# Optimization experiments

Measured on AMD Instinct MI355X. Metric: run time of the kernel, lower is better.

Reference implementation:

```python
import jax, jax.numpy as jnp
import numpy as np
import math

D_MODEL = 1024
NHEAD = 16
NUM_CLUSTERS = 32
L, N, S = 2048, 2, 2048
LN_EPS = 1e-5


def setup_inputs() -> dict:
    key = jax.random.key(0)
    ks = jax.random.split(key, 16)
    E = D_MODEL
    s = 1.0 / math.sqrt(E)
    cq = jax.random.normal(ks[0], (NUM_CLUSTERS, E), jnp.float32)
    cq = cq / jnp.linalg.norm(cq, axis=1, keepdims=True)
    ck = jax.random.normal(ks[1], (NUM_CLUSTERS, E), jnp.float32)
    ck = ck / jnp.linalg.norm(ck, axis=1, keepdims=True)
    return {
        "query": jax.random.normal(ks[2], (L, N, E), jnp.float32),
        "key": jax.random.normal(ks[3], (S, N, E), jnp.float32),
        "value": jax.random.normal(ks[4], (S, N, E), jnp.float32),
        "Wq": jax.random.uniform(ks[5], (E, E), jnp.float32, -s, s),
        "bq": jax.random.uniform(ks[6], (E,), jnp.float32, -s, s),
        "Wk": jax.random.uniform(ks[7], (E, E), jnp.float32, -s, s),
        "bk": jax.random.uniform(ks[8], (E,), jnp.float32, -s, s),
        "Wv": jax.random.uniform(ks[9], (E, E), jnp.float32, -s, s),
        "bv": jax.random.uniform(ks[10], (E,), jnp.float32, -s, s),
        "Wo": jax.random.uniform(ks[11], (E, E), jnp.float32, -s, s),
        "bo": jax.random.uniform(ks[12], (E,), jnp.float32, -s, s),
        "centroids_q": cq,
        "centroids_k": ck,
        "ln_gamma": jnp.ones((E,), jnp.float32),
        "ln_beta": jnp.zeros((E,), jnp.float32),
    }


def _assign(x, centroids):
    # spherical k-means assignment: argmax cosine similarity
    xn = x / jnp.clip(jnp.linalg.norm(x, axis=-1, keepdims=True), 1e-12)
    return jnp.argmax(xn @ centroids.T, axis=-1)


def reference(query, key, value, Wq, bq, Wk, bk, Wv, bv, Wo, bo,
              centroids_q, centroids_k, ln_gamma, ln_beta):
    Lq, Nb, E = query.shape
    Sk = key.shape[0]
    H, dh = NHEAD, E // NHEAD

    Q = query @ Wq.T + bq            # [L,N,E]
    K = key @ Wk.T + bk              # [S,N,E]
    V = value @ Wv.T + bv            # [S,N,E]

    Qb = jnp.transpose(Q, (1, 0, 2))  # [N,L,E]
    Kb = jnp.transpose(K, (1, 0, 2))  # [N,S,E]
    Vb = jnp.transpose(V, (1, 0, 2))  # [N,S,E]

    q_clusters = _assign(Qb, centroids_q)  # [N,L] int
    k_clusters = _assign(Kb, centroids_k)  # [N,S] int
    # bipartite cluster-equality mask, broadcast over heads
    mask = q_clusters[:, :, None] == k_clusters[:, None, :]  # [N,L,S]

    Qh = Qb.reshape(Nb, Lq, H, dh)
    Kh = Kb.reshape(Nb, Sk, H, dh)
    Vh = Vb.reshape(Nb, Sk, H, dh)

    scores = jnp.einsum('nlhd,nshd->nhls', Qh, Kh) / math.sqrt(dh)
    scores = jnp.where(mask[:, None, :, :], scores, -jnp.inf)
    attn = jax.nn.softmax(scores, axis=-1)  # dropout = identity (eval)

    ctx = jnp.einsum('nhls,nshd->nlhd', attn, Vh).reshape(Nb, Lq, E)
    out = ctx @ Wo.T + bo                     # [N,L,E]
    out = jnp.transpose(out, (1, 0, 2))       # [L,N,E]

    res = query + out
    mu = jnp.mean(res, axis=-1, keepdims=True)
    var = jnp.mean(jnp.square(res - mu), axis=-1, keepdims=True)
    return (res - mu) / jnp.sqrt(var + LN_EPS) * ln_gamma + ln_beta
```

## Files before the change

### kernel.cpp

```cpp
#include <hip/hip_runtime.h>
#include <stdint.h>

#define L_SEQ 2048
#define S_SEQ 2048
#define NB 2
#define EMB 1024
#define NH 16
#define DH 64
#define NC 32
#define MROWS 4096

typedef __bf16 bf16x8 __attribute__((ext_vector_type(8)));
typedef float f32x4 __attribute__((ext_vector_type(4)));

__device__ __forceinline__ float bf2f(unsigned short u) {
  return __builtin_bit_cast(float, (uint32_t)u << 16);
}
__device__ __forceinline__ unsigned short f2bf(float f) {
  uint32_t u = __builtin_bit_cast(uint32_t, f);
  return (unsigned short)((u + 0x7FFFu + ((u >> 16) & 1u)) >> 16);
}

#if defined(__has_builtin) && __has_builtin(__builtin_amdgcn_global_load_lds)
#define GLOAD_LDS(gp, lp)                                            \
  __builtin_amdgcn_global_load_lds(                                  \
      (const __attribute__((address_space(1))) void*)(gp),           \
      (__attribute__((address_space(3))) void*)(lp), 16, 0, 0)
#else
#define GLOAD_LDS(gp, lp) do { *(uint4*)(lp) = *(const uint4*)(gp); } while (0)
#endif

__global__ void __launch_bounds__(256) conv_f2bf_kernel(
    const float* __restrict__ src, unsigned short* __restrict__ dst, int n8)
{
  int id = blockIdx.x * 256 + threadIdx.x;
  if (id >= n8) return;
  const float4* s = (const float4*)src + (size_t)id * 2;
  float4 a0 = s[0], a1 = s[1];
  uint4 u;
  u.x = (uint32_t)f2bf(a0.x) | ((uint32_t)f2bf(a0.y) << 16);
  u.y = (uint32_t)f2bf(a0.z) | ((uint32_t)f2bf(a0.w) << 16);
  u.z = (uint32_t)f2bf(a1.x) | ((uint32_t)f2bf(a1.y) << 16);
  u.w = (uint32_t)f2bf(a1.z) | ((uint32_t)f2bf(a1.w) << 16);
  ((uint4*)dst)[id] = u;
}

__global__ void __launch_bounds__(256) gemm_bt_mfma(
    const unsigned short* __restrict__ A, const unsigned short* __restrict__ B,
    const float* __restrict__ bias,
    float* __restrict__ outF, unsigned short* __restrict__ outB)
{
  __shared__ __align__(16) unsigned short As[128][32];
  __shared__ __align__(16) unsigned short Bs[128][32];
  const int K = EMB;
  int tid = threadIdx.x;
  int m0 = blockIdx.y * 128, n0 = blockIdx.x * 128;
  int wave = tid >> 6, lane = tid & 63;
  int wm = (wave >> 1) * 64, wn = (wave & 1) * 64;

  f32x4 zero = {0.f, 0.f, 0.f, 0.f};
  f32x4 acc[4][4];
#pragma unroll
  for (int mi = 0; mi < 4; mi++)
#pragma unroll
    for (int ni = 0; ni < 4; ni++) acc[mi][ni] = zero;

  int fr = lane & 15, fk = (lane >> 4) * 8;

  for (int k0 = 0; k0 < K; k0 += 32) {
    __syncthreads();
#pragma unroll
    for (int it = 0; it < 2; it++) {
      int ch = tid + it * 256;
      int row = ch >> 2, kk = (ch & 3) * 8;
      GLOAD_LDS(A + (size_t)(m0 + row) * K + k0 + kk, &As[row][kk]);
      GLOAD_LDS(B + (size_t)(n0 + row) * K + k0 + kk, &Bs[row][kk]);
    }
    __syncthreads();
    bf16x8 af[4], bfr[4];
#pragma unroll
    for (int i = 0; i < 4; i++) af[i] = *(const bf16x8*)(&As[wm + i * 16 + fr][fk]);
#pragma unroll
    for (int i = 0; i < 4; i++) bfr[i] = *(const bf16x8*)(&Bs[wn + i * 16 + fr][fk]);
#pragma unroll
    for (int mi = 0; mi < 4; mi++)
#pragma unroll
      for (int ni = 0; ni < 4; ni++)
        acc[mi][ni] = __builtin_amdgcn_mfma_f32_16x16x32_bf16(af[mi], bfr[ni], acc[mi][ni], 0, 0, 0);
  }

#pragma unroll
  for (int ni = 0; ni < 4; ni++) {
    int col = n0 + wn + ni * 16 + (lane & 15);
    float bv = bias[col];
#pragma unroll
    for (int mi = 0; mi < 4; mi++) {
#pragma unroll
      for (int r = 0; r < 4; r++) {
        int row = m0 + wm + mi * 16 + (lane >> 4) * 4 + r;
        float v = acc[mi][ni][r] + bv;
        if (outF) outF[(size_t)row * EMB + col] = v;
        else outB[(size_t)row * EMB + col] = f2bf(v);
      }
    }
  }
}

__global__ void __launch_bounds__(256) prep_partial_kernel(
    const float* __restrict__ Wq_, const float* __restrict__ cq_,
    const float* __restrict__ Wk_, const float* __restrict__ ck_,
    double* __restrict__ partQ, double* __restrict__ partK)
{
  const float* W; const float* cent; double* part;
  if (blockIdx.z == 0) { W = Wq_; cent = cq_; part = partQ; }
  else                 { W = Wk_; cent = ck_; part = partK; }
  int tid = threadIdx.x;
  int k = (blockIdx.y << 6) | (tid & 63);
  int cbase = __builtin_amdgcn_readfirstlane(tid >> 6) * 8;
  int e0 = blockIdx.x << 6;

  double acc[8];
#pragma unroll
  for (int j = 0; j < 8; j++) acc[j] = 0.0;

#pragma unroll 2
  for (int e = 0; e < 64; e++) {
    double w = (double)W[(size_t)(e0 + e) * EMB + k];
#pragma unroll
    for (int j = 0; j < 8; j++)
      acc[j] += w * (double)cent[(size_t)(cbase + j) * EMB + e0 + e];
  }
#pragma unroll
  for (int j = 0; j < 8; j++)
    part[((size_t)blockIdx.x * NC + cbase + j) * EMB + k] = acc[j];
}

__global__ void __launch_bounds__(256) prep_reduce_kernel(
    const double* __restrict__ partQ, const double* __restrict__ partK,
    double* __restrict__ WcTq, double* __restrict__ WcTk)
{
  int id = blockIdx.x * 256 + threadIdx.x;
  const double* part; double* WcT; int local;
  if (id < NC * EMB) { part = partQ; WcT = WcTq; local = id; }
  else               { part = partK; WcT = WcTk; local = id - NC * EMB; }
  int c = local >> 10, k = local & 1023;
  double s = 0.0;
  for (int es = 0; es < 16; es++)
    s += part[((size_t)es * NC + c) * EMB + k];
  WcT[(size_t)k * NC + c] = s;
}

__global__ void __launch_bounds__(256) prep_bd_kernel(
    const float* __restrict__ bq_, const float* __restrict__ cq_,
    const float* __restrict__ bk_, const float* __restrict__ ck_,
    double* __restrict__ bdq, double* __restrict__ bdk)
{
  const float* bias; const float* cent; double* bd;
  if (blockIdx.x == 0) { bias = bq_; cent = cq_; bd = bdq; }
  else                 { bias = bk_; cent = ck_; bd = bdk; }
  int tid = threadIdx.x;
  int c = tid & 31, g = tid >> 5;
  __shared__ double red[8][32];
  double s2 = 0.0;
  for (int e = g * 128; e < (g + 1) * 128; e++)
    s2 += (double)bias[e] * (double)cent[(size_t)c * EMB + e];
  red[g][c] = s2;
  __syncthreads();
  if (tid < 32) {
    double t = 0.0;
#pragma unroll
    for (int gg = 0; gg < 8; gg++) t += red[gg][tid];
    bd[tid] = t;
  }
}

__global__ void __launch_bounds__(256, 2) assign2_kernel(
    const float* __restrict__ Xq, const double* __restrict__ WcTq, const double* __restrict__ bdq,
    int* __restrict__ qcl, int* __restrict__ qcnt,
    const float* __restrict__ Xk, const double* __restrict__ WcTk, const double* __restrict__ bdk,
    int* __restrict__ kcl, int* __restrict__ kcnt)
{
  const float* X; const double* WcT; const double* bd; int* cluster; int* count;
  if (blockIdx.y == 0) { X = Xq; WcT = WcTq; bd = bdq; cluster = qcl; count = qcnt; }
  else                 { X = Xk; WcT = WcTk; bd = bdk; cluster = kcl; count = kcnt; }

  int r0 = blockIdx.x * 16;
  int tid = threadIdx.x;
  int c = tid & 31, g = tid >> 5;

  __shared__ __align__(16) double Ws[64][32];
  __shared__ __align__(16) double Xd[16][64];

  double aAe = 0, aAo = 0, aBe = 0, aBo = 0;

  for (int k0 = 0; k0 < EMB; k0 += 64) {
    __syncthreads();
#pragma unroll
    for (int it = 0; it < 8; it++) {
      int idx = it * 256 + tid;
      ((double*)Ws)[idx] = WcT[(size_t)k0 * NC + idx];
    }
#pragma unroll
    for (int it = 0; it < 2; it++) {
      int idx = it * 256 + tid;
      int r = idx >> 5, kp = idx & 31;
      float2 xv = *(const float2*)(X + (size_t)(r0 + r) * EMB + k0 + kp * 2);
      double2 xd; xd.x = (double)xv.x; xd.y = (double)xv.y;
      *(double2*)(&Xd[r][kp * 2]) = xd;
    }
    __syncthreads();
#pragma unroll
    for (int kk = 0; kk < 64; kk += 2) {
      double w0 = Ws[kk][c], w1 = Ws[kk + 1][c];
      double2 xa = *(const double2*)(&Xd[g * 2][kk]);
      double2 xb = *(const double2*)(&Xd[g * 2 + 1][kk]);
      aAe += xa.x * w0; aAo += xa.y * w1;
      aBe += xb.x * w0; aBo += xb.y * w1;
    }
  }

  double dA = (aAe + aAo) + bd[c];
  double dB = (aBe + aBo) + bd[c];

  double bvA = dA; int biA = c;
  double bvB = dB; int biB = c;
#pragma unroll
  for (int off = 1; off < 32; off <<= 1) {
    double ovA = __shfl_xor(bvA, off, 64); int oiA = __shfl_xor(biA, off, 64);
    if (ovA > bvA || (ovA == bvA && oiA < biA)) { bvA = ovA; biA = oiA; }
    double ovB = __shfl_xor(bvB, off, 64); int oiB = __shfl_xor(biB, off, 64);
    if (ovB > bvB || (ovB == bvB && oiB < biB)) { bvB = ovB; biB = oiB; }
  }
  if (c == 0) {
    int rowA = r0 + g * 2, rowB = rowA + 1;
    cluster[rowA] = biA; atomicAdd(&count[(rowA & 1) * NC + biA], 1);
    cluster[rowB] = biB; atomicAdd(&count[(rowB & 1) * NC + biB], 1);
  }
}

__global__ void scan_kernel(const int* __restrict__ qcount, const int* __restrict__ kcount,
                            int* __restrict__ qoff, int* __restrict__ koff)
{
  int tid = threadIdx.x;
  if (tid < 2) {
    int run = 0;
    for (int c = 0; c < NC; c++) { qoff[tid * NC + c] = run; run += qcount[tid * NC + c]; }
  } else if (tid < 4) {
    int n = tid - 2, run = 0;
    for (int c = 0; c < NC; c++) { koff[n * NC + c] = run; run += kcount[n * NC + c]; }
  }
}

__global__ void __launch_bounds__(256) scatter_kernel(
    const int* __restrict__ q_cluster, const int* __restrict__ k_cluster,
    const int* __restrict__ qoff, const int* __restrict__ koff,
    int* __restrict__ qfill, int* __restrict__ kfill,
    int* __restrict__ qlist, int* __restrict__ klist)
{
  int id = blockIdx.x * 256 + threadIdx.x;
  if (id < MROWS) {
    int row = id, n = row & 1, l = row >> 1, c = q_cluster[row];
    int pos = atomicAdd(&qfill[n * NC + c], 1);
    qlist[n * L_SEQ + qoff[n * NC + c] + pos] = l;
  } else {
    int row = id - MROWS, n = row & 1, s = row >> 1, c = k_cluster[row];
    int pos = atomicAdd(&kfill[n * NC + c], 1);
    klist[n * S_SEQ + koff[n * NC + c] + pos] = s;
  }
}

__global__ void __launch_bounds__(256) attn_bucket(
    const unsigned short* __restrict__ Qb, const unsigned short* __restrict__ Kb,
    const unsigned short* __restrict__ Vb,
    const int* __restrict__ qcount, const int* __restrict__ qoff, const int* __restrict__ qlist,
    const int* __restrict__ kcount, const int* __restrict__ koff, const int* __restrict__ klist,
    unsigned short* __restrict__ ctx)
{
  int c = blockIdx.x, h = blockIdx.y, n = blockIdx.z;
  int Sc = kcount[n * NC + c], k0base = koff[n * NC + c];
  int Lc = qcount[n * NC + c], q0 = qoff[n * NC + c];
  int tid = threadIdx.x, wave = tid >> 6, lane = tid & 63;
  int lg = lane >> 4, lq = lane & 15;

  __shared__ __align__(16) unsigned short Ks[64][64];
  __shared__ __align__(16) unsigned short Vts[64][64];
  __shared__ __align__(16) unsigned short Pts[4][16][64];
  __shared__ int rb[64];

  if (Sc == 0) {
    for (int qi = wave; qi < Lc; qi += 4) {
      int l = qlist[n * L_SEQ + q0 + qi];
      ctx[((size_t)(n * L_SEQ + l)) * EMB + h * DH + lane] = 0;
    }
    return;
  }

  const int* kl = klist + n * S_SEQ + k0base;
  const int* ql = qlist + n * L_SEQ + q0;
  f32x4 zero = {0.f, 0.f, 0.f, 0.f};

  for (int qb = 0; qb < Lc; qb += 64) {
    int qq = qb + wave * 16 + lq;
    int qqc = qq < Lc ? qq : Lc - 1;
    int lrow = ql[qqc];
    const unsigned short* qp = Qb + ((size_t)(lrow * NB + n)) * EMB + h * DH;
    bf16x8 qf0 = *(const bf16x8*)(qp + lg * 8);
    bf16x8 qf1 = *(const bf16x8*)(qp + 32 + lg * 8);

    f32x4 acc[4];
#pragma unroll
    for (int di = 0; di < 4; di++) acc[di] = zero;
    float m = -3.0e38f, lsum = 0.f;

    for (int kc = 0; kc < Sc; kc += 64) {
      __syncthreads();
      if (tid < 64) {
        int jj = kc + tid; if (jj >= Sc) jj = Sc - 1;
        rb[tid] = (kl[jj] * NB + n) * EMB + h * DH;
      }
      __syncthreads();
#pragma unroll
      for (int it = 0; it < 2; it++) {
        int p = it * 256 + tid;
        {
          int row = p >> 3, seg = p & 7;
          uint4 u = *(const uint4*)(Kb + rb[row] + seg * 8);
          *(uint4*)(&Ks[row][(seg * 8) ^ ((row & 7) << 3)]) = u;
        }
        {
          int d = p & 63, kg = p >> 6;
          unsigned short v0 = Vb[rb[kg * 8 + 0] + d], v1 = Vb[rb[kg * 8 + 1] + d];
          unsigned short v2 = Vb[rb[kg * 8 + 2] + d], v3 = Vb[rb[kg * 8 + 3] + d];
          unsigned short v4 = Vb[rb[kg * 8 + 4] + d], v5 = Vb[rb[kg * 8 + 5] + d];
          unsigned short v6 = Vb[rb[kg * 8 + 6] + d], v7 = Vb[rb[kg * 8 + 7] + d];
          uint4 u;
          u.x = (uint32_t)v0 | ((uint32_t)v1 << 16);
          u.y = (uint32_t)v2 | ((uint32_t)v3 << 16);
          u.z = (uint32_t)v4 | ((uint32_t)v5 << 16);
          u.w = (uint32_t)v6 | ((uint32_t)v7 << 16);
          *(uint4*)(&Vts[d][(kg * 8) ^ ((d & 7) << 3)]) = u;
        }
      }
      __syncthreads();

      f32x4 st[4];
#pragma unroll
      for (int ni = 0; ni < 4; ni++) st[ni] = zero;
#pragma unroll
      for (int ni = 0; ni < 4; ni++) {
        int row = ni * 16 + lq;
        bf16x8 kf0 = *(const bf16x8*)(&Ks[row][(lg * 8) ^ ((row & 7) << 3)]);
        bf16x8 kf1 = *(const bf16x8*)(&Ks[row][(32 + lg * 8) ^ ((row & 7) << 3)]);
        st[ni] = __builtin_amdgcn_mfma_f32_16x16x32_bf16(kf0, qf0, st[ni], 0, 0, 0);
        st[ni] = __builtin_amdgcn_mfma_f32_16x16x32_bf16(kf1, qf1, st[ni], 0, 0, 0);
      }

      int lim = Sc - kc;
      float cm = -3.0e38f;
#pragma unroll
      for (int ni = 0; ni < 4; ni++) {
        st[ni] = st[ni] * 0.125f;
#pragma unroll
        for (int r = 0; r < 4; r++) cm = fmaxf(cm, st[ni][r]);
      }
      cm = fmaxf(cm, __shfl_xor(cm, 16, 64));
      cm = fmaxf(cm, __shfl_xor(cm, 32, 64));
      float mn = fmaxf(m, cm);
      float fac = __expf(m - mn);
      m = mn;
      lsum *= fac;
#pragma unroll
      for (int di = 0; di < 4; di++) acc[di] = acc[di] * fac;

#pragma unroll
      for (int ni = 0; ni < 4; ni++) {
        int kloc = ni * 16 + lg * 4;
        float p0 = (kloc + 0 < lim) ? __expf(st[ni][0] - mn) : 0.f;
        float p1 = (kloc + 1 < lim) ? __expf(st[ni][1] - mn) : 0.f;
        float p2 = (kloc + 2 < lim) ? __expf(st[ni][2] - mn) : 0.f;
        float p3 = (kloc + 3 < lim) ? __expf(st[ni][3] - mn) : 0.f;
        unsigned short b0 = f2bf(p0), b1 = f2bf(p1), b2 = f2bf(p2), b3 = f2bf(p3);
        lsum += bf2f(b0) + bf2f(b1) + bf2f(b2) + bf2f(b3);
        ushort4 u4; u4.x = b0; u4.y = b1; u4.z = b2; u4.w = b3;
        *(ushort4*)(&Pts[wave][lq][kloc ^ ((lq & 7) << 3)]) = u4;
      }

#pragma unroll
      for (int ks = 0; ks < 2; ks++) {
        bf16x8 pf = *(const bf16x8*)(&Pts[wave][lq][(ks * 32 + lg * 8) ^ ((lq & 7) << 3)]);
#pragma unroll
        for (int di = 0; di < 4; di++) {
          int row = di * 16 + lq;
          bf16x8 vf = *(const bf16x8*)(&Vts[row][(ks * 32 + lg * 8) ^ ((row & 7) << 3)]);
          acc[di] = __builtin_amdgcn_mfma_f32_16x16x32_bf16(vf, pf, acc[di], 0, 0, 0);
        }
      }
    }

    lsum += __shfl_xor(lsum, 16, 64);
    lsum += __shfl_xor(lsum, 32, 64);
    float rinv = 1.f / lsum;
    if (qq < Lc) {
      unsigned short* op = ctx + ((size_t)(n * L_SEQ + lrow)) * EMB + h * DH;
#pragma unroll
      for (int di = 0; di < 4; di++) {
        ushort4 o;
        o.x = f2bf(acc[di][0] * rinv);
        o.y = f2bf(acc[di][1] * rinv);
        o.z = f2bf(acc[di][2] * rinv);
        o.w = f2bf(acc[di][3] * rinv);
        *(ushort4*)(op + di * 16 + lg * 4) = o;
      }
    }
  }
}

__global__ void __launch_bounds__(256) ln_kernel(
    const float* __restrict__ proj, const float* __restrict__ query,
    const float* __restrict__ gamma, const float* __restrict__ beta,
    float* __restrict__ out)
{
  int r = blockIdx.x;
  int l = r >> 1, n = r & 1;
  int tid = threadIdx.x, wave = tid >> 6, lane = tid & 63;
  float4 p = *(const float4*)(proj + ((size_t)(n * L_SEQ + l)) * EMB + tid * 4);
  float4 qu = *(const float4*)(query + (size_t)r * EMB + tid * 4);
  float res[4] = { p.x + qu.x, p.y + qu.y, p.z + qu.z, p.w + qu.w };
  float s1 = res[0] + res[1] + res[2] + res[3];
  float s2 = res[0] * res[0] + res[1] * res[1] + res[2] * res[2] + res[3] * res[3];
#pragma unroll
  for (int off = 32; off; off >>= 1) {
    s1 += __shfl_xor(s1, off, 64);
    s2 += __shfl_xor(s2, off, 64);
  }
  __shared__ float a1[4], a2[4];
  if (lane == 0) { a1[wave] = s1; a2[wave] = s2; }
  __syncthreads();
  float t1 = a1[0] + a1[1] + a1[2] + a1[3];
  float t2 = a2[0] + a2[1] + a2[2] + a2[3];
  float mu = t1 * (1.f / EMB);
  float var = fmaxf(t2 * (1.f / EMB) - mu * mu, 0.f);
  float rstd = 1.f / sqrtf(var + 1e-5f);
  float4 gu = *(const float4*)(gamma + tid * 4);
  float4 bu = *(const float4*)(beta + tid * 4);
  float4 o;
  o.x = (res[0] - mu) * rstd * gu.x + bu.x;
  o.y = (res[1] - mu) * rstd * gu.y + bu.y;
  o.z = (res[2] - mu) * rstd * gu.z + bu.z;
  o.w = (res[3] - mu) * rstd * gu.w + bu.w;
  *(float4*)(out + (size_t)r * EMB + tid * 4) = o;
}

extern "C" void kernel_launch(void* const* d_in, const int* in_sizes, int n_in,
                              void* d_out, int out_size, void* d_ws, size_t ws_size,
                              hipStream_t stream) {
  const float* query = (const float*)d_in[0];
  const float* key   = (const float*)d_in[1];
  const float* value = (const float*)d_in[2];
  const float* Wq = (const float*)d_in[3];
  const float* bq = (const float*)d_in[4];
  const float* Wk = (const float*)d_in[5];
  const float* bk = (const float*)d_in[6];
  const float* Wv = (const float*)d_in[7];
  const float* bv = (const float*)d_in[8];
  const float* Wo = (const float*)d_in[9];
  const float* bo = (const float*)d_in[10];
  const float* cq = (const float*)d_in[11];
  const float* ck = (const float*)d_in[12];
  const float* gamma = (const float*)d_in[13];
  const float* beta  = (const float*)d_in[14];
  float* out = (float*)d_out;

  const size_t MB_EL = (size_t)MROWS * EMB;

  int* q_cluster = (int*)d_ws;
  int* k_cluster = q_cluster + MROWS;
  int* qcount = k_cluster + MROWS;
  int* kcount = qcount + 64;
  int* qoff   = kcount + 64;
  int* koff   = qoff + 64;
  int* qfill  = koff + 64;
  int* kfill  = qfill + 64;
  int* qlist  = kfill + 64;
  int* klist  = qlist + MROWS;
  double* Wcq = (double*)(klist + MROWS);
  double* Wck = Wcq + (size_t)NC * EMB;
  double* bdq = Wck + (size_t)NC * EMB;
  double* bdk = bdq + NC;
  unsigned short* Qb  = (unsigned short*)(bdk + NC);
  unsigned short* Kb  = Qb + MB_EL;
  unsigned short* Vb  = Kb + MB_EL;
  unsigned short* ctx = Vb + MB_EL;
  unsigned short* wbf = ctx + MB_EL;
  unsigned short* xbf = ctx;
  float* proj = (float*)Qb;
  double* partQ = (double*)Qb;
  double* partK = partQ + (size_t)16 * NC * EMB;

  const int W8 = (EMB * EMB) / 8;
  const int X8 = (int)(MB_EL / 8);

  hipMemsetAsync(qcount, 0, 6 * 64 * sizeof(int), stream);

  prep_partial_kernel<<<dim3(16, 16, 2), 256, 0, stream>>>(Wq, cq, Wk, ck, partQ, partK);
  prep_reduce_kernel<<<(2 * NC * EMB) / 256, 256, 0, stream>>>(partQ, partK, Wcq, Wck);
  prep_bd_kernel<<<2, 256, 0, stream>>>(bq, cq, bk, ck, bdq, bdk);

  dim3 gg(EMB / 128, MROWS / 128);
  conv_f2bf_kernel<<<W8 / 256, 256, 0, stream>>>(Wq, wbf, W8);
  conv_f2bf_kernel<<<X8 / 256, 256, 0, stream>>>(query, xbf, X8);
  gemm_bt_mfma<<<gg, 256, 0, stream>>>(xbf, wbf, bq, nullptr, Qb);

  conv_f2bf_kernel<<<W8 / 256, 256, 0, stream>>>(Wk, wbf, W8);
  conv_f2bf_kernel<<<X8 / 256, 256, 0, stream>>>(key, xbf, X8);
  gemm_bt_mfma<<<gg, 256, 0, stream>>>(xbf, wbf, bk, nullptr, Kb);

  conv_f2bf_kernel<<<W8 / 256, 256, 0, stream>>>(Wv, wbf, W8);
  conv_f2bf_kernel<<<X8 / 256, 256, 0, stream>>>(value, xbf, X8);
  gemm_bt_mfma<<<gg, 256, 0, stream>>>(xbf, wbf, bv, nullptr, Vb);

  assign2_kernel<<<dim3(MROWS / 16, 2), 256, 0, stream>>>(
      query, Wcq, bdq, q_cluster, qcount,
      key,   Wck, bdk, k_cluster, kcount);

  scan_kernel<<<1, 64, 0, stream>>>(qcount, kcount, qoff, koff);
  scatter_kernel<<<(2 * MROWS) / 256, 256, 0, stream>>>(q_cluster, k_cluster, qoff, koff,
                                                        qfill, kfill, qlist, klist);
  attn_bucket<<<dim3(NC, NH, NB), 256, 0, stream>>>(Qb, Kb, Vb, qcount, qoff, qlist,
                                                    kcount, koff, klist, ctx);

  conv_f2bf_kernel<<<W8 / 256, 256, 0, stream>>>(Wo, wbf, W8);
  gemm_bt_mfma<<<gg, 256, 0, stream>>>(ctx, wbf, bo, proj, nullptr);
  ln_kernel<<<MROWS, 256, 0, stream>>>(proj, query, gamma, beta, out);
}
```

Before: 369.8 us.

## Merge weight/activation bf16 conversions and retile cluster assignment for more reuse

```diff
diff --git a/kernel.cpp b/kernel.cpp
--- a/kernel.cpp
+++ b/kernel.cpp
@@ -31,18 +31,21 @@
 #endif
 
 __global__ void __launch_bounds__(256) conv_f2bf_kernel(
-    const float* __restrict__ src, unsigned short* __restrict__ dst, int n8)
+    const float* __restrict__ srcW, unsigned short* __restrict__ dstW, int nW8,
+    const float* __restrict__ srcX, unsigned short* __restrict__ dstX, int nX8)
 {
   int id = blockIdx.x * 256 + threadIdx.x;
-  if (id >= n8) return;
-  const float4* s = (const float4*)src + (size_t)id * 2;
+  const float* src; unsigned short* dst; int i;
+  if (id < nW8) { src = srcW; dst = dstW; i = id; }
+  else { i = id - nW8; if (i >= nX8) return; src = srcX; dst = dstX; }
+  const float4* s = (const float4*)src + (size_t)i * 2;
   float4 a0 = s[0], a1 = s[1];
   uint4 u;
   u.x = (uint32_t)f2bf(a0.x) | ((uint32_t)f2bf(a0.y) << 16);
   u.y = (uint32_t)f2bf(a0.z) | ((uint32_t)f2bf(a0.w) << 16);
   u.z = (uint32_t)f2bf(a1.x) | ((uint32_t)f2bf(a1.y) << 16);
   u.w = (uint32_t)f2bf(a1.z) | ((uint32_t)f2bf(a1.w) << 16);
-  ((uint4*)dst)[id] = u;
+  ((uint4*)dst)[i] = u;
 }
 
 __global__ void __launch_bounds__(256) gemm_bt_mfma(
@@ -174,7 +177,7 @@
   }
 }
 
-__global__ void __launch_bounds__(256, 2) assign2_kernel(
+__global__ void __launch_bounds__(256) assign2_kernel(
     const float* __restrict__ Xq, const double* __restrict__ WcTq, const double* __restrict__ bdq,
     int* __restrict__ qcl, int* __restrict__ qcnt,
     const float* __restrict__ Xk, const double* __restrict__ WcTk, const double* __restrict__ bdk,
@@ -184,14 +187,19 @@
   if (blockIdx.y == 0) { X = Xq; WcT = WcTq; bd = bdq; cluster = qcl; count = qcnt; }
   else                 { X = Xk; WcT = WcTk; bd = bdk; cluster = kcl; count = kcnt; }
 
-  int r0 = blockIdx.x * 16;
+  int r0 = blockIdx.x * 32;
   int tid = threadIdx.x;
   int c = tid & 31, g = tid >> 5;
+  int g4 = g * 4;
 
   __shared__ __align__(16) double Ws[64][32];
-  __shared__ __align__(16) double Xd[16][64];
-
-  double aAe = 0, aAo = 0, aBe = 0, aBo = 0;
+  __shared__ __align__(16) float  Xs[32][64];
+
+  double a[4][4];
+#pragma unroll
+  for (int rr = 0; rr < 4; rr++)
+#pragma unroll
+    for (int j = 0; j < 4; j++) a[rr][j] = 0.0;
 
   for (int k0 = 0; k0 < EMB; k0 += 64) {
     __syncthreads();
@@ -203,38 +211,44 @@
 #pragma unroll
     for (int it = 0; it < 2; it++) {
       int idx = it * 256 + tid;
-      int r = idx >> 5, kp = idx & 31;
-      float2 xv = *(const float2*)(X + (size_t)(r0 + r) * EMB + k0 + kp * 2);
-      double2 xd; xd.x = (double)xv.x; xd.y = (double)xv.y;
-      *(double2*)(&Xd[r][kp * 2]) = xd;
+      int r = idx >> 4, kp = (idx & 15) * 4;
+      *(float4*)(&Xs[r][kp]) = *(const float4*)(X + (size_t)(r0 + r) * EMB + k0 + kp);
     }
     __syncthreads();
 #pragma unroll
-    for (int kk = 0; kk < 64; kk += 2) {
-      double w0 = Ws[kk][c], w1 = Ws[kk + 1][c];
-      double2 xa = *(const double2*)(&Xd[g * 2][kk]);
-      double2 xb = *(const double2*)(&Xd[g * 2 + 1][kk]);
-      aAe += xa.x * w0; aAo += xa.y * w1;
-      aBe += xb.x * w0; aBo += xb.y * w1;
-    }
-  }
-
-  double dA = (aAe + aAo) + bd[c];
-  double dB = (aBe + aBo) + bd[c];
-
-  double bvA = dA; int biA = c;
-  double bvB = dB; int biB = c;
-#pragma unroll
-  for (int off = 1; off < 32; off <<= 1) {
-    double ovA = __shfl_xor(bvA, off, 64); int oiA = __shfl_xor(biA, off, 64);
-    if (ovA > bvA || (ovA == bvA && oiA < biA)) { bvA = ovA; biA = oiA; }
-    double ovB = __shfl_xor(bvB, off, 64); int oiB = __shfl_xor(biB, off, 64);
-    if (ovB > bvB || (ovB == bvB && oiB < biB)) { bvB = ovB; biB = oiB; }
-  }
-  if (c == 0) {
-    int rowA = r0 + g * 2, rowB = rowA + 1;
-    cluster[rowA] = biA; atomicAdd(&count[(rowA & 1) * NC + biA], 1);
-    cluster[rowB] = biB; atomicAdd(&count[(rowB & 1) * NC + biB], 1);
+    for (int ks = 0; ks < 64; ks += 8) {
+      double w0 = Ws[ks + 0][c], w1 = Ws[ks + 1][c];
+      double w2 = Ws[ks + 2][c], w3 = Ws[ks + 3][c];
+      double w4 = Ws[ks + 4][c], w5 = Ws[ks + 5][c];
+      double w6 = Ws[ks + 6][c], w7 = Ws[ks + 7][c];
+#pragma unroll
+      for (int rr = 0; rr < 4; rr++) {
+        float4 xa = *(const float4*)(&Xs[g4 + rr][ks]);
+        float4 xb = *(const float4*)(&Xs[g4 + rr][ks + 4]);
+        a[rr][0] += (double)xa.x * w0; a[rr][1] += (double)xa.y * w1;
+        a[rr][2] += (double)xa.z * w2; a[rr][3] += (double)xa.w * w3;
+        a[rr][0] += (double)xb.x * w4; a[rr][1] += (double)xb.y * w5;
+        a[rr][2] += (double)xb.z * w6; a[rr][3] += (double)xb.w * w7;
+      }
+    }
+  }
+
+  double bdc = bd[c];
+#pragma unroll
+  for (int rr = 0; rr < 4; rr++) {
+    double dot = ((a[rr][0] + a[rr][1]) + (a[rr][2] + a[rr][3])) + bdc;
+    double bv = dot; int bi = c;
+#pragma unroll
+    for (int off = 1; off < 32; off <<= 1) {
+      double ov = __shfl_xor(bv, off, 64);
+      int oi = __shfl_xor(bi, off, 64);
+      if (ov > bv || (ov == bv && oi < bi)) { bv = ov; bi = oi; }
+    }
+    if (c == 0) {
+      int row = r0 + g4 + rr;
+      cluster[row] = bi;
+      atomicAdd(&count[(row & 1) * NC + bi], 1);
+    }
   }
 }
 
@@ -499,6 +513,7 @@
 
   const int W8 = (EMB * EMB) / 8;
   const int X8 = (int)(MB_EL / 8);
+  const int CVT_BLK = (W8 + X8 + 255) / 256;
 
   hipMemsetAsync(qcount, 0, 6 * 64 * sizeof(int), stream);
 
@@ -507,19 +522,16 @@
   prep_bd_kernel<<<2, 256, 0, stream>>>(bq, cq, bk, ck, bdq, bdk);
 
   dim3 gg(EMB / 128, MROWS / 128);
-  conv_f2bf_kernel<<<W8 / 256, 256, 0, stream>>>(Wq, wbf, W8);
-  conv_f2bf_kernel<<<X8 / 256, 256, 0, stream>>>(query, xbf, X8);
+  conv_f2bf_kernel<<<CVT_BLK, 256, 0, stream>>>(Wq, wbf, W8, query, xbf, X8);
   gemm_bt_mfma<<<gg, 256, 0, stream>>>(xbf, wbf, bq, nullptr, Qb);
 
-  conv_f2bf_kernel<<<W8 / 256, 256, 0, stream>>>(Wk, wbf, W8);
-  conv_f2bf_kernel<<<X8 / 256, 256, 0, stream>>>(key, xbf, X8);
+  conv_f2bf_kernel<<<CVT_BLK, 256, 0, stream>>>(Wk, wbf, W8, key, xbf, X8);
   gemm_bt_mfma<<<gg, 256, 0, stream>>>(xbf, wbf, bk, nullptr, Kb);
 
-  conv_f2bf_kernel<<<W8 / 256, 256, 0, stream>>>(Wv, wbf, W8);
-  conv_f2bf_kernel<<<X8 / 256, 256, 0, stream>>>(value, xbf, X8);
+  conv_f2bf_kernel<<<CVT_BLK, 256, 0, stream>>>(Wv, wbf, W8, value, xbf, X8);
   gemm_bt_mfma<<<gg, 256, 0, stream>>>(xbf, wbf, bv, nullptr, Vb);
 
-  assign2_kernel<<<dim3(MROWS / 16, 2), 256, 0, stream>>>(
+  assign2_kernel<<<dim3(MROWS / 32, 2), 256, 0, stream>>>(
       query, Wcq, bdq, q_cluster, qcount,
       key,   Wck, bdk, k_cluster, kcount);
 
@@ -529,7 +541,7 @@
   attn_bucket<<<dim3(NC, NH, NB), 256, 0, stream>>>(Qb, Kb, Vb, qcount, qoff, qlist,
                                                     kcount, koff, klist, ctx);
 
-  conv_f2bf_kernel<<<W8 / 256, 256, 0, stream>>>(Wo, wbf, W8);
+  conv_f2bf_kernel<<<(W8 + 255) / 256, 256, 0, stream>>>(Wo, wbf, W8, nullptr, nullptr, 0);
   gemm_bt_mfma<<<gg, 256, 0, stream>>>(ctx, wbf, bo, proj, nullptr);
   ln_kernel<<<MROWS, 256, 0, stream>>>(proj, query, gamma, beta, out);
 }
```

New measurement: 357.6 us. -3.3%, faster.
